# Optimization experiments

Measured on AMD Instinct MI355X. Metric: run time of the kernel, lower is better.

Reference implementation:

```python
import jax, jax.numpy as jnp
import numpy as np

B, S, D = 32, 512, 768
H = 12
HD = D // H
SCALE = HD ** -0.5


def setup_inputs() -> dict:
    key = jax.random.key(0)
    ks = jax.random.split(key, 5)
    return {
        "x": jax.random.normal(ks[0], (B, S, D), dtype=jnp.float32),
        "qkv_w": jax.random.normal(ks[1], (3 * D, D), dtype=jnp.float32) * (D ** -0.5),
        "qkv_b": jax.random.normal(ks[2], (3 * D,), dtype=jnp.float32) * 0.02,
        "proj_w": jax.random.normal(ks[3], (D, D), dtype=jnp.float32) * (D ** -0.5),
        "proj_b": jax.random.normal(ks[4], (D,), dtype=jnp.float32) * 0.02,
    }


def reference(x, qkv_w, qkv_b, proj_w, proj_b) -> jnp.ndarray:
    b, s, d = x.shape
    # fused QKV projection (torch Linear: x @ W.T + b)
    qkv = x @ qkv_w.T + qkv_b                      # [B,S,3D]
    qkv = qkv.reshape(b, s, 3, H, HD)
    qkv = jnp.transpose(qkv, (2, 0, 3, 1, 4))      # [3,B,H,S,HD]
    q, k, v = qkv[0], qkv[1], qkv[2]
    scores = jnp.einsum("bhqd,bhkd->bhqk", q, k) * SCALE  # [B,H,S,S]
    # attn_drop with p=0.0 (eval) -> identity
    attn = jax.nn.softmax(scores, axis=-1)
    out = jnp.einsum("bhqk,bhkd->bhqd", attn, v)   # [B,H,S,HD]
    out = jnp.transpose(out, (0, 2, 1, 3)).reshape(b, s, d)
    out = out @ proj_w.T + proj_b                  # proj_drop p=0.0 -> identity
    return out
```

## Files before the change

kernel.cpp:

```cpp
#include <hip/hip_runtime.h>
#include <hip/hip_bf16.h>

#define B_  32
#define S_  512
#define D_  768
#define H_  12
#define HD_ 64
#define QKV_ELEMS (B_ * H_ * S_ * HD_)

typedef __hip_bfloat16 bf16;
typedef short bf16x8_t __attribute__((ext_vector_type(8)));
typedef float f32x4_t  __attribute__((ext_vector_type(4)));

__device__ __forceinline__ float bf2f(bf16 x) { return __bfloat162float(x); }
__device__ __forceinline__ bf16  f2bf(float x) { return __float2bfloat16(x); }

__device__ __forceinline__ void gl_lds16(const short* g, short* l) {
    __builtin_amdgcn_global_load_lds(
        (const __attribute__((address_space(1))) void*)g,
        (__attribute__((address_space(3))) void*)l, 16, 0, 0);
}

__global__ __launch_bounds__(256) void f2bf_kernel(
    const float* __restrict__ in, unsigned short* __restrict__ out, int n4)
{
    int i = blockIdx.x * 256 + threadIdx.x;
    if (i >= n4) return;
    float4 v = reinterpret_cast<const float4*>(in)[i];
    ushort4 o;
    o.x = __bfloat16_as_ushort(f2bf(v.x));
    o.y = __bfloat16_as_ushort(f2bf(v.y));
    o.z = __bfloat16_as_ushort(f2bf(v.z));
    o.w = __bfloat16_as_ushort(f2bf(v.w));
    reinterpret_cast<ushort4*>(out)[i] = o;
}

#define GEMM_CORE(As, Bs, Aptr, Bptr, m0, n0, K)                               \
    const int t = threadIdx.x;                                                 \
    const int w = t >> 6, lane = t & 63;                                       \
    const int wr = w >> 1, wc = w & 1;                                         \
    const int quad = lane >> 4, l16 = lane & 15;                               \
    f32x4_t acc[4][4] = {};                                                    \
    const int lrow = lane >> 3;                                                \
    const int scol = (((lane & 7) ^ (lrow & 7)) * 8);                          \
    _Pragma("unroll")                                                          \
    for (int j = 0; j < 4; ++j) {                                              \
        int R = j * 32 + w * 8;                                                \
        gl_lds16((Aptr) + (size_t)((m0) + R + lrow) * (K) + scol, &(As)[R * 64]); \
        gl_lds16((Bptr) + (size_t)((n0) + R + lrow) * (K) + scol, &(Bs)[R * 64]); \
    }                                                                          \
    for (int k0 = 0; k0 < (K); k0 += 64) {                                     \
        const int curo = ((k0 >> 6) & 1) * 8192;                               \
        __syncthreads();                                                       \
        if (k0 + 64 < (K)) {                                                   \
            const int nxo = curo ^ 8192;                                       \
            _Pragma("unroll")                                                  \
            for (int j = 0; j < 4; ++j) {                                      \
                int R = j * 32 + w * 8;                                        \
                gl_lds16((Aptr) + (size_t)((m0) + R + lrow) * (K) + k0 + 64 + scol, \
                         &(As)[nxo + R * 64]);                                 \
                gl_lds16((Bptr) + (size_t)((n0) + R + lrow) * (K) + k0 + 64 + scol, \
                         &(Bs)[nxo + R * 64]);                                 \
            }                                                                  \
        }                                                                      \
        _Pragma("unroll")                                                      \
        for (int ks = 0; ks < 64; ks += 32) {                                  \
            bf16x8_t af[4], bf_[4];                                            \
            _Pragma("unroll")                                                  \
            for (int tm = 0; tm < 4; ++tm)                                     \
                af[tm] = *(const bf16x8_t*)&(As)[curo + (wr * 64 + tm * 16 + l16) * 64 \
                        + ((((ks >> 3) + quad) ^ (l16 & 7)) * 8)];             \
            _Pragma("unroll")                                                  \
            for (int tn = 0; tn < 4; ++tn)                                     \
                bf_[tn] = *(const bf16x8_t*)&(Bs)[curo + (wc * 64 + tn * 16 + l16) * 64 \
                        + ((((ks >> 3) + quad) ^ (l16 & 7)) * 8)];             \
            _Pragma("unroll")                                                  \
            for (int tm = 0; tm < 4; ++tm)                                     \
                _Pragma("unroll")                                              \
                for (int tn = 0; tn < 4; ++tn)                                 \
                    acc[tm][tn] = __builtin_amdgcn_mfma_f32_16x16x32_bf16(     \
                        af[tm], bf_[tn], acc[tm][tn], 0, 0, 0);                \
        }                                                                      \
    }

__global__ __launch_bounds__(256) void qkv_gemm_mfma(
    const short* __restrict__ A, const short* __restrict__ W,
    const float* __restrict__ bias,
    bf16* __restrict__ Q, bf16* __restrict__ Kp, bf16* __restrict__ Vp)
{
    __shared__ short As[2 * 128 * 64];
    __shared__ short Bs[2 * 128 * 64];
    const int n0 = blockIdx.x * 128;
    const int m0 = blockIdx.y * 128;
    GEMM_CORE(As, Bs, A, W, m0, n0, 768)

    const int which = n0 / 768;
    const int h = ((n0 + wc * 64) % 768) >> 6;
    bf16* dst = (which == 0) ? Q : (which == 1) ? Kp : Vp;
    float bv[4];
#pragma unroll
    for (int tn = 0; tn < 4; ++tn) bv[tn] = bias[n0 + wc * 64 + tn * 16 + l16];
#pragma unroll
    for (int tm = 0; tm < 4; ++tm) {
#pragma unroll
        for (int r = 0; r < 4; ++r) {
            int m = m0 + wr * 64 + tm * 16 + quad * 4 + r;
            int b = m >> 9, s = m & 511;
            size_t rb = (((size_t)b * H_ + h) * S_ + s) * HD_;
#pragma unroll
            for (int tn = 0; tn < 4; ++tn)
                dst[rb + tn * 16 + l16] = f2bf(acc[tm][tn][r] + bv[tn]);
        }
    }
}

__global__ __launch_bounds__(256) void proj_gemm_mfma(
    const short* __restrict__ A, const short* __restrict__ W,
    const float* __restrict__ bias, float* __restrict__ out)
{
    __shared__ short As[2 * 128 * 64];
    __shared__ short Bs[2 * 128 * 64];
    const int n0 = blockIdx.x * 128;
    const int m0 = blockIdx.y * 128;
    GEMM_CORE(As, Bs, A, W, m0, n0, 768)

    float bv[4];
#pragma unroll
    for (int tn = 0; tn < 4; ++tn) bv[tn] = bias[n0 + wc * 64 + tn * 16 + l16];
#pragma unroll
    for (int tm = 0; tm < 4; ++tm) {
#pragma unroll
        for (int r = 0; r < 4; ++r) {
            int m = m0 + wr * 64 + tm * 16 + quad * 4 + r;
#pragma unroll
            for (int tn = 0; tn < 4; ++tn)
                out[(size_t)m * 768 + n0 + wc * 64 + tn * 16 + l16] =
                    acc[tm][tn][r] + bv[tn];
        }
    }
}

#define QT 128
#define KT 64
#define PS 68
#define VS 68

__global__ __launch_bounds__(256, 3) void attn_mfma(
    const short* __restrict__ Qg, const short* __restrict__ Kg,
    const short* __restrict__ Vg, bf16* __restrict__ O)
{
    __shared__ short Qs[QT * 64];
    __shared__ short Ks[KT * 64];
    __shared__ short Vt[64 * VS];
    __shared__ short Ps[QT * PS];

    const int t = threadIdx.x;
    const int w = t >> 6, lane = t & 63;
    const int quad = lane >> 4, l16 = lane & 15;
    const int lrow = lane >> 3;
    const int scol = (((lane & 7) ^ (lrow & 7)) * 8);
    const int qt = blockIdx.x & 3;
    const int bh = blockIdx.x >> 2;
    const int q0 = qt * QT;
    const size_t base = (size_t)bh * (S_ * HD_);

#pragma unroll
    for (int j = 0; j < 4; ++j) {
        int R = j * 32 + w * 8;
        gl_lds16(Qg + base + (size_t)(q0 + R + lrow) * 64 + scol, &Qs[R * 64]);
    }

    const int wq = w * 32;
    f32x4_t Oacc[2][4] = {};
    float lsum[2][4] = {};

    for (int kt = 0; kt < S_; kt += KT) {
        __syncthreads();
#pragma unroll
        for (int j = 0; j < 2; ++j) {
            int R = j * 32 + w * 8;
            gl_lds16(Kg + base + (size_t)(kt + R + lrow) * 64 + scol, &Ks[R * 64]);
        }
        {
            int k = lane, dg = w;
            const bf16x8_t* gv = (const bf16x8_t*)(Vg + base + (size_t)(kt + k) * 64 + dg * 16);
            bf16x8_t v0 = gv[0], v1 = gv[1];
#pragma unroll
            for (int i = 0; i < 8; ++i) {
                Vt[(dg * 16 + i) * VS + k]     = v0[i];
                Vt[(dg * 16 + 8 + i) * VS + k] = v1[i];
            }
        }
        __syncthreads();

        f32x4_t sc[2][4] = {};
#pragma unroll
        for (int ks = 0; ks < 64; ks += 32) {
            bf16x8_t aq[2], bk[4];
#pragma unroll
            for (int tm = 0; tm < 2; ++tm)
                aq[tm] = *(const bf16x8_t*)&Qs[(wq + tm * 16 + l16) * 64
                        + ((((ks >> 3) + quad) ^ (l16 & 7)) * 8)];
#pragma unroll
            for (int tn = 0; tn < 4; ++tn)
                bk[tn] = *(const bf16x8_t*)&Ks[(tn * 16 + l16) * 64
                        + ((((ks >> 3) + quad) ^ (l16 & 7)) * 8)];
#pragma unroll
            for (int tm = 0; tm < 2; ++tm)
#pragma unroll
                for (int tn = 0; tn < 4; ++tn)
                    sc[tm][tn] = __builtin_amdgcn_mfma_f32_16x16x32_bf16(
                        aq[tm], bk[tn], sc[tm][tn], 0, 0, 0);
        }

#pragma unroll
        for (int tm = 0; tm < 2; ++tm) {
#pragma unroll
            for (int r = 0; r < 4; ++r) {
                int row = wq + tm * 16 + quad * 4 + r;
                float rs = 0.f;
#pragma unroll
                for (int tn = 0; tn < 4; ++tn) {
                    float p = __expf(sc[tm][tn][r] * 0.125f);
                    rs += p;
                    Ps[row * PS + tn * 16 + l16] = (short)__bfloat16_as_ushort(f2bf(p));
                }
                lsum[tm][r] += rs;
            }
        }

#pragma unroll
        for (int ks = 0; ks < 64; ks += 32) {
            bf16x8_t ap[2], bv[4];
#pragma unroll
            for (int tm = 0; tm < 2; ++tm)
                ap[tm] = *(const bf16x8_t*)&Ps[(wq + tm * 16 + l16) * PS + ks + quad * 8];
#pragma unroll
            for (int tn = 0; tn < 4; ++tn)
                bv[tn] = *(const bf16x8_t*)&Vt[(tn * 16 + l16) * VS + ks + quad * 8];
#pragma unroll
            for (int tm = 0; tm < 2; ++tm)
#pragma unroll
                for (int tn = 0; tn < 4; ++tn)
                    Oacc[tm][tn] = __builtin_amdgcn_mfma_f32_16x16x32_bf16(
                        ap[tm], bv[tn], Oacc[tm][tn], 0, 0, 0);
        }
    }

    float linv[2][4];
#pragma unroll
    for (int tm = 0; tm < 2; ++tm)
#pragma unroll
        for (int r = 0; r < 4; ++r) {
            float v = lsum[tm][r];
            v += __shfl_xor(v, 1, 64);
            v += __shfl_xor(v, 2, 64);
            v += __shfl_xor(v, 4, 64);
            v += __shfl_xor(v, 8, 64);
            linv[tm][r] = 1.f / v;
        }
    const int b = bh / H_, h = bh % H_;
#pragma unroll
    for (int tm = 0; tm < 2; ++tm) {
#pragma unroll
        for (int r = 0; r < 4; ++r) {
            int row = q0 + wq + tm * 16 + quad * 4 + r;
            size_t ob = ((size_t)b * S_ + row) * D_ + h * HD_;
#pragma unroll
            for (int tn = 0; tn < 4; ++tn)
                O[ob + tn * 16 + l16] = f2bf(Oacc[tm][tn][r] * linv[tm][r]);
        }
    }
}

extern "C" void kernel_launch(void* const* d_in, const int* in_sizes, int n_in,
                              void* d_out, int out_size, void* d_ws, size_t ws_size,
                              hipStream_t stream) {
    const float* x      = (const float*)d_in[0];
    const float* qkv_w  = (const float*)d_in[1];
    const float* qkv_b  = (const float*)d_in[2];
    const float* proj_w = (const float*)d_in[3];
    const float* proj_b = (const float*)d_in[4];
    float* out = (float*)d_out;

    unsigned short* q     = (unsigned short*)d_ws;
    unsigned short* k     = q + QKV_ELEMS;
    unsigned short* v     = k + QKV_ELEMS;
    unsigned short* slot4 = v + QKV_ELEMS;
    unsigned short* wq    = slot4 + QKV_ELEMS;
    unsigned short* wp    = wq + 2304 * 768;

    f2bf_kernel<<<(16384 * 768 / 4 + 255) / 256, 256, 0, stream>>>(x, slot4, 16384 * 768 / 4);
    f2bf_kernel<<<(2304 * 768 / 4 + 255) / 256, 256, 0, stream>>>(qkv_w, wq, 2304 * 768 / 4);
    f2bf_kernel<<<(768 * 768 / 4 + 255) / 256, 256, 0, stream>>>(proj_w, wp, 768 * 768 / 4);

    qkv_gemm_mfma<<<dim3(18, 128), 256, 0, stream>>>(
        (const short*)slot4, (const short*)wq, qkv_b,
        (bf16*)q, (bf16*)k, (bf16*)v);

    attn_mfma<<<dim3(32 * 12 * 4), 256, 0, stream>>>(
        (const short*)q, (const short*)k, (const short*)v, (bf16*)slot4);

    proj_gemm_mfma<<<dim3(6, 128), 256, 0, stream>>>(
        (const short*)slot4, (const short*)wp, proj_b, out);
}
```

Baseline: 285.1 us.

## Rewrite GEMMs as 256x256 tiles with 8 waves and phased async pipeline

Replaces the 128x128, 4-wave GEMM core used by the QKV and output projections with a 256x256 tile computed by 8 waves. The K loop is split into four phases per step, each interleaving half-tile global-to-LDS staging with MFMA bursts. It uses explicit vmcnt waits, raw barriers and s_setprio, and adds an XCD-aware block swizzle on a 1D grid. The goal is more data reuse per tile and better overlap of loads with matrix math. In exchange it uses much more LDS and more registers per block, and the hand-tuned wait counts must exactly match the outstanding loads or the result is wrong.

```diff
diff --git a/kernel.cpp b/kernel.cpp
--- a/kernel.cpp
+++ b/kernel.cpp
@@ -35,76 +35,110 @@
     reinterpret_cast<ushort4*>(out)[i] = o;
 }
 
-#define GEMM_CORE(As, Bs, Aptr, Bptr, m0, n0, K)                               \
+#define VM6() asm volatile("s_waitcnt vmcnt(6)" ::: "memory")
+#define VM0() asm volatile("s_waitcnt vmcnt(0)" ::: "memory")
+#define BAR() do { asm volatile("" ::: "memory"); \
+                   __builtin_amdgcn_s_barrier(); \
+                   asm volatile("" ::: "memory"); } while (0)
+
+#define STAGE_HALF(Ls, gp, grow0, kcol, hoff) do {                             \
+    const int g0_ = (hoff) + w * 8;                                            \
+    gl_lds16((gp) + (size_t)((grow0) + g0_ + lrow) * 768 + (kcol) + scol,      \
+             (Ls) + g0_ * 64);                                                 \
+    const int g1_ = 128 + (hoff) + w * 8;                                      \
+    gl_lds16((gp) + (size_t)((grow0) + g1_ + lrow) * 768 + (kcol) + scol,      \
+             (Ls) + g1_ * 64);                                                 \
+  } while (0)
+
+#define RD_A(i0)                                                               \
+    _Pragma("unroll") for (int th = 0; th < 2; ++th)                           \
+      _Pragma("unroll") for (int ks = 0; ks < 2; ++ks)                         \
+        afr[th][ks] = *(const bf16x8_t*)&As[cb                                 \
+            + (wr * 128 + ((i0) * 2 + th) * 16 + l16) * 64                     \
+            + (((ks * 4 + quad) ^ (l16 & 7)) * 8)]
+
+#define PH_MFMA(i0)                                                            \
+    __builtin_amdgcn_s_setprio(1);                                             \
+    _Pragma("unroll") for (int th = 0; th < 2; ++th)                           \
+      _Pragma("unroll") for (int tn = 0; tn < 4; ++tn)                         \
+        _Pragma("unroll") for (int ks = 0; ks < 2; ++ks)                       \
+          acc[(i0) * 2 + th][tn] = __builtin_amdgcn_mfma_f32_16x16x32_bf16(    \
+              afr[th][ks], bfr[tn][ks], acc[(i0) * 2 + th][tn], 0, 0, 0);      \
+    __builtin_amdgcn_s_setprio(0)
+
+#define GEMM256_CORE(Aptr, Bptr, NBN)                                          \
+    __shared__ short As[2 * 256 * 64];                             \
+    __shared__ short Bs[2 * 256 * 64];                             \
+    const int bid = blockIdx.x;                                                \
+      \
+      \
+    const int swz = (bid & 7) * ((int)gridDim.x >> 3) + (bid >> 3);            \
+    const int m0 = (swz / (NBN)) * 256;                                        \
+    const int n0 = (swz % (NBN)) * 256;                                        \
     const int t = threadIdx.x;                                                 \
     const int w = t >> 6, lane = t & 63;                                       \
-    const int wr = w >> 1, wc = w & 1;                                         \
+    const int wr = w >> 2, wc = w & 3;                                         \
     const int quad = lane >> 4, l16 = lane & 15;                               \
-    f32x4_t acc[4][4] = {};                                                    \
     const int lrow = lane >> 3;                                                \
-    const int scol = (((lane & 7) ^ (lrow & 7)) * 8);                          \
-    _Pragma("unroll")                                                          \
-    for (int j = 0; j < 4; ++j) {                                              \
-        int R = j * 32 + w * 8;                                                \
-        gl_lds16((Aptr) + (size_t)((m0) + R + lrow) * (K) + scol, &(As)[R * 64]); \
-        gl_lds16((Bptr) + (size_t)((n0) + R + lrow) * (K) + scol, &(Bs)[R * 64]); \
-    }                                                                          \
-    for (int k0 = 0; k0 < (K); k0 += 64) {                                     \
-        const int curo = ((k0 >> 6) & 1) * 8192;                               \
-        __syncthreads();                                                       \
-        if (k0 + 64 < (K)) {                                                   \
-            const int nxo = curo ^ 8192;                                       \
-            _Pragma("unroll")                                                  \
-            for (int j = 0; j < 4; ++j) {                                      \
-                int R = j * 32 + w * 8;                                        \
-                gl_lds16((Aptr) + (size_t)((m0) + R + lrow) * (K) + k0 + 64 + scol, \
-                         &(As)[nxo + R * 64]);                                 \
-                gl_lds16((Bptr) + (size_t)((n0) + R + lrow) * (K) + k0 + 64 + scol, \
-                         &(Bs)[nxo + R * 64]);                                 \
-            }                                                                  \
-        }                                                                      \
-        _Pragma("unroll")                                                      \
-        for (int ks = 0; ks < 64; ks += 32) {                                  \
-            bf16x8_t af[4], bf_[4];                                            \
-            _Pragma("unroll")                                                  \
-            for (int tm = 0; tm < 4; ++tm)                                     \
-                af[tm] = *(const bf16x8_t*)&(As)[curo + (wr * 64 + tm * 16 + l16) * 64 \
-                        + ((((ks >> 3) + quad) ^ (l16 & 7)) * 8)];             \
-            _Pragma("unroll")                                                  \
-            for (int tn = 0; tn < 4; ++tn)                                     \
-                bf_[tn] = *(const bf16x8_t*)&(Bs)[curo + (wc * 64 + tn * 16 + l16) * 64 \
-                        + ((((ks >> 3) + quad) ^ (l16 & 7)) * 8)];             \
-            _Pragma("unroll")                                                  \
-            for (int tm = 0; tm < 4; ++tm)                                     \
-                _Pragma("unroll")                                              \
-                for (int tn = 0; tn < 4; ++tn)                                 \
-                    acc[tm][tn] = __builtin_amdgcn_mfma_f32_16x16x32_bf16(     \
-                        af[tm], bf_[tn], acc[tm][tn], 0, 0, 0);                \
-        }                                                                      \
-    }
-
-__global__ __launch_bounds__(256) void qkv_gemm_mfma(
+    const int scol = ((lane & 7) ^ lrow) * 8;                                  \
+    f32x4_t acc[8][4] = {};                                                    \
+     \
+    STAGE_HALF(&As[0],     Aptr, m0, 0,  0);                                   \
+    STAGE_HALF(&As[0],     Aptr, m0, 0,  64);                                  \
+    STAGE_HALF(&Bs[0],     Bptr, n0, 0,  0);                                   \
+    STAGE_HALF(&Bs[0],     Bptr, n0, 0,  64);                                  \
+    STAGE_HALF(&Bs[16384], Bptr, n0, 64, 0);                                   \
+    STAGE_HALF(&Bs[16384], Bptr, n0, 64, 64);                                  \
+    STAGE_HALF(&As[16384], Aptr, m0, 64, 0);                                   \
+    VM6(); BAR();   \
+    for (int tt = 0; tt < 12; ++tt) {                                          \
+      const int cb = (tt & 1) << 14;                                           \
+      const int ob = cb ^ 16384;                                               \
+      const int kc1 = (tt + 1) << 6, kc2 = (tt + 2) << 6;                      \
+      bf16x8_t bfr[4][2], afr[2][2];                                           \
+                                                        \
+      if (tt < 11) STAGE_HALF(&As[ob], Aptr, m0, kc1, 64);                     \
+      _Pragma("unroll") for (int tn = 0; tn < 4; ++tn)                         \
+        _Pragma("unroll") for (int ks = 0; ks < 2; ++ks)                       \
+          bfr[tn][ks] = *(const bf16x8_t*)&Bs[cb                               \
+              + (wc * 64 + tn * 16 + l16) * 64                                 \
+              + (((ks * 4 + quad) ^ (l16 & 7)) * 8)];                          \
+      RD_A(0);                                                                 \
+      BAR(); PH_MFMA(0); BAR();                                                \
+                                                        \
+      if (tt < 10) STAGE_HALF(&Bs[cb], Bptr, n0, kc2, 0);                      \
+      RD_A(1);                                                                 \
+      BAR(); PH_MFMA(1); BAR();                                                \
+                                                        \
+      if (tt < 10) STAGE_HALF(&Bs[cb], Bptr, n0, kc2, 64);                     \
+      RD_A(2);                                                                 \
+      BAR(); PH_MFMA(2); BAR();                                                \
+                                                        \
+      if (tt < 10) STAGE_HALF(&As[cb], Aptr, m0, kc2, 0);                      \
+      RD_A(3);                                                                 \
+      BAR(); PH_MFMA(3);                                                       \
+      if (tt == 10) { VM0(); } else if (tt < 10) { VM6(); }                    \
+      BAR();                                                                   \
+    }
+
+__global__ __launch_bounds__(512, 2) void qkv_gemm_mfma(
     const short* __restrict__ A, const short* __restrict__ W,
     const float* __restrict__ bias,
     bf16* __restrict__ Q, bf16* __restrict__ Kp, bf16* __restrict__ Vp)
 {
-    __shared__ short As[2 * 128 * 64];
-    __shared__ short Bs[2 * 128 * 64];
-    const int n0 = blockIdx.x * 128;
-    const int m0 = blockIdx.y * 128;
-    GEMM_CORE(As, Bs, A, W, m0, n0, 768)
+    GEMM256_CORE(A, W, 9)
 
     const int which = n0 / 768;
-    const int h = ((n0 + wc * 64) % 768) >> 6;
+    const int h = ((n0 % 768) >> 6) + wc;
     bf16* dst = (which == 0) ? Q : (which == 1) ? Kp : Vp;
     float bv[4];
 #pragma unroll
     for (int tn = 0; tn < 4; ++tn) bv[tn] = bias[n0 + wc * 64 + tn * 16 + l16];
 #pragma unroll
-    for (int tm = 0; tm < 4; ++tm) {
+    for (int tm = 0; tm < 8; ++tm) {
 #pragma unroll
         for (int r = 0; r < 4; ++r) {
-            int m = m0 + wr * 64 + tm * 16 + quad * 4 + r;
+            int m = m0 + wr * 128 + tm * 16 + quad * 4 + r;
             int b = m >> 9, s = m & 511;
             size_t rb = (((size_t)b * H_ + h) * S_ + s) * HD_;
 #pragma unroll
@@ -114,24 +148,20 @@
     }
 }
 
-__global__ __launch_bounds__(256) void proj_gemm_mfma(
+__global__ __launch_bounds__(512, 2) void proj_gemm_mfma(
     const short* __restrict__ A, const short* __restrict__ W,
     const float* __restrict__ bias, float* __restrict__ out)
 {
-    __shared__ short As[2 * 128 * 64];
-    __shared__ short Bs[2 * 128 * 64];
-    const int n0 = blockIdx.x * 128;
-    const int m0 = blockIdx.y * 128;
-    GEMM_CORE(As, Bs, A, W, m0, n0, 768)
+    GEMM256_CORE(A, W, 3)
 
     float bv[4];
 #pragma unroll
     for (int tn = 0; tn < 4; ++tn) bv[tn] = bias[n0 + wc * 64 + tn * 16 + l16];
 #pragma unroll
-    for (int tm = 0; tm < 4; ++tm) {
+    for (int tm = 0; tm < 8; ++tm) {
 #pragma unroll
         for (int r = 0; r < 4; ++r) {
-            int m = m0 + wr * 64 + tm * 16 + quad * 4 + r;
+            int m = m0 + wr * 128 + tm * 16 + quad * 4 + r;
 #pragma unroll
             for (int tn = 0; tn < 4; ++tn)
                 out[(size_t)m * 768 + n0 + wc * 64 + tn * 16 + l16] =
@@ -294,13 +324,13 @@
     f2bf_kernel<<<(2304 * 768 / 4 + 255) / 256, 256, 0, stream>>>(qkv_w, wq, 2304 * 768 / 4);
     f2bf_kernel<<<(768 * 768 / 4 + 255) / 256, 256, 0, stream>>>(proj_w, wp, 768 * 768 / 4);
 
-    qkv_gemm_mfma<<<dim3(18, 128), 256, 0, stream>>>(
+    qkv_gemm_mfma<<<dim3(64 * 9), 512, 0, stream>>>(
         (const short*)slot4, (const short*)wq, qkv_b,
         (bf16*)q, (bf16*)k, (bf16*)v);
 
     attn_mfma<<<dim3(32 * 12 * 4), 256, 0, stream>>>(
         (const short*)q, (const short*)k, (const short*)v, (bf16*)slot4);
 
-    proj_gemm_mfma<<<dim3(6, 128), 256, 0, stream>>>(
+    proj_gemm_mfma<<<dim3(64 * 3), 512, 0, stream>>>(
         (const short*)slot4, (const short*)wp, proj_b, out);
 }
```

Result: slower. 317.9 us (+11.5%).

## Double-buffer K/V tiles in attention, keep Q in registers, remap blocks

Applied to the files above, without the earlier changes.

The attention kernel now double-buffers the K and V LDS tiles, prefetching the next tile (K via direct-to-LDS loads, V into registers and then transposed into LDS) while the current tile is computed, which cuts one barrier per iteration. Q fragments are loaded once from global straight into registers, removing the Q LDS buffer. The block index mapping is changed so neighbouring blocks cover different heads, and s_setprio is raised around the MFMA sections. LDS use grows with the second K/V buffer and more live registers may hurt occupancy at 3 blocks per CU.

```diff
diff --git a/kernel.cpp b/kernel.cpp
--- a/kernel.cpp
+++ b/kernel.cpp
@@ -149,9 +149,8 @@
     const short* __restrict__ Qg, const short* __restrict__ Kg,
     const short* __restrict__ Vg, bf16* __restrict__ O)
 {
-    __shared__ short Qs[QT * 64];
-    __shared__ short Ks[KT * 64];
-    __shared__ short Vt[64 * VS];
+    __shared__ short Ks[2][KT * 64];
+    __shared__ short Vt[2][64 * VS];
     __shared__ short Ps[QT * PS];
 
     const int t = threadIdx.x;
@@ -159,59 +158,72 @@
     const int quad = lane >> 4, l16 = lane & 15;
     const int lrow = lane >> 3;
     const int scol = (((lane & 7) ^ (lrow & 7)) * 8);
-    const int qt = blockIdx.x & 3;
-    const int bh = blockIdx.x >> 2;
+    const int bid = blockIdx.x;
+    const int bh = (bid & 7) + 8 * (bid >> 5);
+    const int qt = (bid >> 3) & 3;
     const int q0 = qt * QT;
     const size_t base = (size_t)bh * (S_ * HD_);
-
-#pragma unroll
-    for (int j = 0; j < 4; ++j) {
-        int R = j * 32 + w * 8;
-        gl_lds16(Qg + base + (size_t)(q0 + R + lrow) * 64 + scol, &Qs[R * 64]);
-    }
-
     const int wq = w * 32;
+
+    bf16x8_t aq[2][2];
+#pragma unroll
+    for (int tm = 0; tm < 2; ++tm)
+#pragma unroll
+        for (int ksi = 0; ksi < 2; ++ksi)
+            aq[tm][ksi] = *(const bf16x8_t*)(Qg + base
+                + (size_t)(q0 + wq + tm * 16 + l16) * 64 + ksi * 32 + quad * 8);
+
     f32x4_t Oacc[2][4] = {};
     float lsum[2][4] = {};
 
-    for (int kt = 0; kt < S_; kt += KT) {
-        __syncthreads();
-#pragma unroll
-        for (int j = 0; j < 2; ++j) {
-            int R = j * 32 + w * 8;
-            gl_lds16(Kg + base + (size_t)(kt + R + lrow) * 64 + scol, &Ks[R * 64]);
-        }
-        {
-            int k = lane, dg = w;
-            const bf16x8_t* gv = (const bf16x8_t*)(Vg + base + (size_t)(kt + k) * 64 + dg * 16);
-            bf16x8_t v0 = gv[0], v1 = gv[1];
-#pragma unroll
-            for (int i = 0; i < 8; ++i) {
-                Vt[(dg * 16 + i) * VS + k]     = v0[i];
-                Vt[(dg * 16 + 8 + i) * VS + k] = v1[i];
+#pragma unroll
+    for (int j = 0; j < 2; ++j) {
+        int R = j * 32 + w * 8;
+        gl_lds16(Kg + base + (size_t)(R + lrow) * 64 + scol, &Ks[0][R * 64]);
+    }
+    {
+        const bf16x8_t* gv = (const bf16x8_t*)(Vg + base + (size_t)lane * 64 + w * 16);
+        bf16x8_t v0 = gv[0], v1 = gv[1];
+#pragma unroll
+        for (int i = 0; i < 8; ++i) {
+            Vt[0][(w * 16 + i) * VS + lane]     = v0[i];
+            Vt[0][(w * 16 + 8 + i) * VS + lane] = v1[i];
+        }
+    }
+    __syncthreads();
+
+    for (int kt = 0; kt < 8; ++kt) {
+        const int cur = kt & 1, nxt = cur ^ 1;
+        bf16x8_t pv0 = {}, pv1 = {};
+        if (kt < 7) {
+#pragma unroll
+            for (int j = 0; j < 2; ++j) {
+                int R = j * 32 + w * 8;
+                gl_lds16(Kg + base + (size_t)((kt + 1) * KT + R + lrow) * 64 + scol,
+                         &Ks[nxt][R * 64]);
             }
-        }
-        __syncthreads();
+            const bf16x8_t* gv = (const bf16x8_t*)(Vg + base
+                + (size_t)((kt + 1) * KT + lane) * 64 + w * 16);
+            pv0 = gv[0]; pv1 = gv[1];
+        }
 
         f32x4_t sc[2][4] = {};
+        __builtin_amdgcn_s_setprio(1);
 #pragma unroll
         for (int ks = 0; ks < 64; ks += 32) {
-            bf16x8_t aq[2], bk[4];
-#pragma unroll
-            for (int tm = 0; tm < 2; ++tm)
-                aq[tm] = *(const bf16x8_t*)&Qs[(wq + tm * 16 + l16) * 64
-                        + ((((ks >> 3) + quad) ^ (l16 & 7)) * 8)];
-#pragma unroll
-            for (int tn = 0; tn < 4; ++tn)
-                bk[tn] = *(const bf16x8_t*)&Ks[(tn * 16 + l16) * 64
+            bf16x8_t bk[4];
+#pragma unroll
+            for (int tn = 0; tn < 4; ++tn)
+                bk[tn] = *(const bf16x8_t*)&Ks[cur][(tn * 16 + l16) * 64
                         + ((((ks >> 3) + quad) ^ (l16 & 7)) * 8)];
 #pragma unroll
             for (int tm = 0; tm < 2; ++tm)
 #pragma unroll
                 for (int tn = 0; tn < 4; ++tn)
                     sc[tm][tn] = __builtin_amdgcn_mfma_f32_16x16x32_bf16(
-                        aq[tm], bk[tn], sc[tm][tn], 0, 0, 0);
-        }
+                        aq[tm][ks >> 5], bk[tn], sc[tm][tn], 0, 0, 0);
+        }
+        __builtin_amdgcn_s_setprio(0);
 
 #pragma unroll
         for (int tm = 0; tm < 2; ++tm) {
@@ -229,6 +241,7 @@
             }
         }
 
+        __builtin_amdgcn_s_setprio(1);
 #pragma unroll
         for (int ks = 0; ks < 64; ks += 32) {
             bf16x8_t ap[2], bv[4];
@@ -237,7 +250,7 @@
                 ap[tm] = *(const bf16x8_t*)&Ps[(wq + tm * 16 + l16) * PS + ks + quad * 8];
 #pragma unroll
             for (int tn = 0; tn < 4; ++tn)
-                bv[tn] = *(const bf16x8_t*)&Vt[(tn * 16 + l16) * VS + ks + quad * 8];
+                bv[tn] = *(const bf16x8_t*)&Vt[cur][(tn * 16 + l16) * VS + ks + quad * 8];
 #pragma unroll
             for (int tm = 0; tm < 2; ++tm)
 #pragma unroll
@@ -245,6 +258,16 @@
                     Oacc[tm][tn] = __builtin_amdgcn_mfma_f32_16x16x32_bf16(
                         ap[tm], bv[tn], Oacc[tm][tn], 0, 0, 0);
         }
+        __builtin_amdgcn_s_setprio(0);
+
+        if (kt < 7) {
+#pragma unroll
+            for (int i = 0; i < 8; ++i) {
+                Vt[nxt][(w * 16 + i) * VS + lane]     = pv0[i];
+                Vt[nxt][(w * 16 + 8 + i) * VS + lane] = pv1[i];
+            }
+        }
+        __syncthreads();
     }
 
     float linv[2][4];
```

After: 276.0 us. 3.2% less time.
